# Kernel tuning notes

Measured on AMD Instinct MI355X. Metric: run time of the kernel, lower is better.

Reference implementation:

```python
import jax, jax.numpy as jnp
import numpy as np

V, BLOCK, L, H, E = 1000, 1024, 8, 16, 1024
D = E // H
HID = 4 * E
B, S = 4, 1024
NEG = -1e9


def setup_inputs() -> dict:
    key = jax.random.key(0)
    ks = jax.random.split(key, 10)
    s = 0.02
    rn = lambda k, shp: jax.random.normal(k, shp, jnp.float32) * s
    return dict(
        idx=jax.random.randint(ks[0], (B, S), 0, V),
        wte=rn(ks[1], (V, E)),
        wpe=rn(ks[2], (BLOCK, E)),
        ln1_w=jnp.ones((L, E), jnp.float32), ln1_b=jnp.zeros((L, E), jnp.float32),
        qkv_w=rn(ks[3], (L, E, 3 * E)), qkv_b=jnp.zeros((L, 3 * E), jnp.float32),
        out_w=rn(ks[4], (L, E, E)), out_b=jnp.zeros((L, E), jnp.float32),
        ln2_w=jnp.ones((L, E), jnp.float32), ln2_b=jnp.zeros((L, E), jnp.float32),
        fc1_w=rn(ks[5], (L, E, HID)), fc1_b=jnp.zeros((L, HID), jnp.float32),
        fc2_w=rn(ks[6], (L, HID, E)), fc2_b=jnp.zeros((L, E), jnp.float32),
        lnf_w=jnp.ones((E,), jnp.float32), lnf_b=jnp.zeros((E,), jnp.float32),
        head_w=rn(ks[7], (E, V)), head_b=jnp.zeros((V,), jnp.float32),
    )


def _ln(x, w, b):
    m = x.mean(-1, keepdims=True)
    v = x.var(-1, keepdims=True)
    return (x - m) / jnp.sqrt(v + 1e-5) * w + b


def _block(x, p):
    (ln1_w, ln1_b, qkv_w, qkv_b, out_w, out_b,
     ln2_w, ln2_b, fc1_w, fc1_b, fc2_w, fc2_b) = p
    b, s, _ = x.shape
    # --- causal self-attention ---
    h = _ln(x, ln1_w, ln1_b)
    qkv = h @ qkv_w + qkv_b                           # [b, s, 3E]
    q, k, v = jnp.split(qkv, 3, axis=-1)
    q = q.reshape(b, s, H, D)
    k = k.reshape(b, s, H, D)
    v = v.reshape(b, s, H, D)
    att = jnp.einsum('bqhd,bkhd->bhqk', q, k) / np.sqrt(D).astype(np.float32)
    mask = jnp.tril(jnp.ones((s, s), bool))
    att = jnp.where(mask, att, NEG)
    att = jax.nn.softmax(att, axis=-1)
    y = jnp.einsum('bhqk,bkhd->bqhd', att, v).reshape(b, s, E)
    x = x + (y @ out_w + out_b)
    # --- MLP ---
    h = _ln(x, ln2_w, ln2_b)
    h = jax.nn.gelu(h @ fc1_w + fc1_b, approximate=False)
    x = x + (h @ fc2_w + fc2_b)
    return x


def reference(idx, wte, wpe, ln1_w, ln1_b, qkv_w, qkv_b, out_w, out_b,
              ln2_w, ln2_b, fc1_w, fc1_b, fc2_w, fc2_b, lnf_w, lnf_b,
              head_w, head_b):
    s = idx.shape[1]
    x = wte[idx] + wpe[:s]                            # [B, S, E]
    layer_params = (ln1_w, ln1_b, qkv_w, qkv_b, out_w, out_b,
                    ln2_w, ln2_b, fc1_w, fc1_b, fc2_w, fc2_b)
    def step(x, p):
        return _block(x, p), None
    x, _ = jax.lax.scan(step, x, layer_params)
    x = _ln(x, lnf_w, lnf_b)
    logits = x @ head_w + head_b                      # [B, S, V]
    return logits
```

## Files before the change

### kernel.cpp

```cpp
#include <hip/hip_runtime.h>
#include <math.h>


typedef unsigned short u16;
typedef unsigned int u32;
typedef __attribute__((ext_vector_type(4))) float f32x4;
typedef __attribute__((ext_vector_type(8))) __bf16 bf16x8;
typedef __attribute__((ext_vector_type(8))) u16 u16x8;
typedef __attribute__((ext_vector_type(4))) u16 u16x4;

#define E 1024
#define HID 4096
#define NH 16
#define HD 64
#define SEQ 1024
#define NB 4
#define NL 8
#define MTOK 4096
#define VOC 1000

#define VMCNT(n) asm volatile("s_waitcnt vmcnt(" #n ")" ::: "memory")

__device__ __forceinline__ u16 f2bf(float f){
  u32 u = __float_as_uint(f);
  u32 r = (u + 0x7fffu + ((u >> 16) & 1u)) >> 16;
  return (u16)r;
}
__device__ __forceinline__ float bf2f(u16 b){
  return __uint_as_float((u32)b << 16);
}
__device__ __forceinline__ bf16x8 ld_bf8(const u16* p){
  return *reinterpret_cast<const bf16x8*>(p);
}
__device__ __forceinline__ bf16x8 as_bf(u16x8 v){
  return __builtin_bit_cast(bf16x8, v);
}

__device__ __forceinline__ void gload16(const void* g, void* l){
  __builtin_amdgcn_global_load_lds(
      (const __attribute__((address_space(1))) void*)g,
      (__attribute__((address_space(3))) void*)l, 16, 0, 0);
}

__global__ __launch_bounds__(256) void embed_kernel(
    const int* __restrict__ idx, const float* __restrict__ wte,
    const float* __restrict__ wpe, u16* __restrict__ x)
{
  int tok = blockIdx.x, tid = threadIdx.x;
  int id = idx[tok];
  int s = tok & (SEQ - 1);
  f32x4 a = *reinterpret_cast<const f32x4*>(&wte[(size_t)id * E + tid * 4]);
  f32x4 p = *reinterpret_cast<const f32x4*>(&wpe[(size_t)s * E + tid * 4]);
  u16x4 r;
  #pragma unroll
  for (int j = 0; j < 4; j++) r[j] = f2bf(a[j] + p[j]);
  *reinterpret_cast<u16x4*>(&x[(size_t)tok * E + tid * 4]) = r;
}

__global__ __launch_bounds__(256) void ln_kernel(
    const u16* __restrict__ x, const float* __restrict__ w,
    const float* __restrict__ b, u16* __restrict__ h)
{
  int row = blockIdx.x, tid = threadIdx.x;
  u16x4 xv = *reinterpret_cast<const u16x4*>(&x[(size_t)row * E + tid * 4]);
  f32x4 v;
  #pragma unroll
  for (int j = 0; j < 4; j++) v[j] = bf2f(xv[j]);
  float s = v[0] + v[1] + v[2] + v[3];
  float q = v[0]*v[0] + v[1]*v[1] + v[2]*v[2] + v[3]*v[3];
  #pragma unroll
  for (int mm = 1; mm < 64; mm <<= 1){
    s += __shfl_xor(s, mm);
    q += __shfl_xor(q, mm);
  }
  __shared__ float red[8];
  int wv = tid >> 6;
  if ((tid & 63) == 0){ red[wv] = s; red[4 + wv] = q; }
  __syncthreads();
  s = red[0] + red[1] + red[2] + red[3];
  q = red[4] + red[5] + red[6] + red[7];
  float mean = s * (1.0f / E);
  float var = q * (1.0f / E) - mean * mean;
  float rstd = rsqrtf(var + 1e-5f);
  f32x4 wv4 = *reinterpret_cast<const f32x4*>(w + tid * 4);
  f32x4 bv4 = *reinterpret_cast<const f32x4*>(b + tid * 4);
  u16x4 o;
  #pragma unroll
  for (int j = 0; j < 4; j++)
    o[j] = f2bf((v[j] - mean) * rstd * wv4[j] + bv4[j]);
  *reinterpret_cast<u16x4*>(&h[(size_t)row * E + tid * 4]) = o;
}

__global__ __launch_bounds__(256) void lnadd_kernel(
    u16* __restrict__ x, const u16* __restrict__ p,
    const float* __restrict__ w, const float* __restrict__ b,
    u16* __restrict__ h)
{
  int row = blockIdx.x, tid = threadIdx.x;
  u16* xr = x + (size_t)row * E + tid * 4;
  u16x4 xv = *reinterpret_cast<const u16x4*>(xr);
  u16x4 pv = *reinterpret_cast<const u16x4*>(&p[(size_t)row * E + tid * 4]);
  f32x4 v;
  u16x4 nx;
  #pragma unroll
  for (int j = 0; j < 4; j++){
    v[j] = bf2f(xv[j]) + bf2f(pv[j]);
    nx[j] = f2bf(v[j]);
  }
  *reinterpret_cast<u16x4*>(xr) = nx;
  float s = v[0] + v[1] + v[2] + v[3];
  float q = v[0]*v[0] + v[1]*v[1] + v[2]*v[2] + v[3]*v[3];
  #pragma unroll
  for (int mm = 1; mm < 64; mm <<= 1){
    s += __shfl_xor(s, mm);
    q += __shfl_xor(q, mm);
  }
  __shared__ float red[8];
  int wv = tid >> 6;
  if ((tid & 63) == 0){ red[wv] = s; red[4 + wv] = q; }
  __syncthreads();
  s = red[0] + red[1] + red[2] + red[3];
  q = red[4] + red[5] + red[6] + red[7];
  float mean = s * (1.0f / E);
  float var = q * (1.0f / E) - mean * mean;
  float rstd = rsqrtf(var + 1e-5f);
  f32x4 wv4 = *reinterpret_cast<const f32x4*>(w + tid * 4);
  f32x4 bv4 = *reinterpret_cast<const f32x4*>(b + tid * 4);
  u16x4 o;
  #pragma unroll
  for (int j = 0; j < 4; j++)
    o[j] = f2bf((v[j] - mean) * rstd * wv4[j] + bv4[j]);
  *reinterpret_cast<u16x4*>(&h[(size_t)row * E + tid * 4]) = o;
}

__global__ __launch_bounds__(256) void wconv4_kernel(
    const float* __restrict__ qw, const float* __restrict__ ow,
    const float* __restrict__ f1, const float* __restrict__ f2,
    u16* __restrict__ dq, u16* __restrict__ d_unused, u16* __restrict__ d1,
    u16* __restrict__ d2, u16* __restrict__ dw_out)
{
  const int bid = blockIdx.x, tid = threadIdx.x;
  const float* W; u16* Wt; int K, Nsrc, nx, base;
  if (bid < 768)      { W = qw; Wt = dq;     K = 1024; Nsrc = 3072; nx = 48; base = 0; }
  else if (bid < 1024){ W = ow; Wt = dw_out; K = 1024; Nsrc = 1024; nx = 16; base = 768; }
  else if (bid < 2048){ W = f1; Wt = d1;     K = 1024; Nsrc = 4096; nx = 64; base = 1024; }
  else                { W = f2; Wt = d2;     K = 4096; Nsrc = 1024; nx = 16; base = 2048; }
  const int t = bid - base;
  const int n0 = (t % nx) * 64, k0 = (t / nx) * 64;

  __shared__ float T[64][65];
  const int c = (tid & 15) * 4, rbase = tid >> 4;
  #pragma unroll
  for (int p = 0; p < 4; p++){
    int r = rbase + p * 16;
    f32x4 v = *reinterpret_cast<const f32x4*>(&W[(size_t)(k0 + r) * Nsrc + n0 + c]);
    T[r][c] = v[0]; T[r][c+1] = v[1]; T[r][c+2] = v[2]; T[r][c+3] = v[3];
  }
  __syncthreads();
  const int nr = tid >> 2, ks = (tid & 3) * 16;
  u16x8 o0, o1;
  #pragma unroll
  for (int i = 0; i < 8; i++){
    o0[i] = f2bf(T[ks + i][nr]);
    o1[i] = f2bf(T[ks + 8 + i][nr]);
  }
  u16* dst = &Wt[(size_t)(n0 + nr) * K + k0 + ks];
  *reinterpret_cast<u16x8*>(dst) = o0;
  *reinterpret_cast<u16x8*>(dst + 8) = o1;
}

__global__ __launch_bounds__(256) void wconv_kernel(
    const float* __restrict__ W, u16* __restrict__ Wt,
    int K, int Nsrc, int N)
{
  __shared__ float T[64][65];
  const int tid = threadIdx.x;
  const int n0 = blockIdx.x * 64, k0 = blockIdx.y * 64;
  const int c = (tid & 15) * 4, rbase = tid >> 4;
  #pragma unroll
  for (int p = 0; p < 4; p++){
    int r = rbase + p * 16;
    #pragma unroll
    for (int j = 0; j < 4; j++){
      int n = n0 + c + j;
      T[r][c + j] = (n < Nsrc) ? W[(size_t)(k0 + r) * Nsrc + n] : 0.0f;
    }
  }
  __syncthreads();
  const int nr = tid >> 2, ks = (tid & 3) * 16;
  u16x8 o0, o1;
  #pragma unroll
  for (int i = 0; i < 8; i++){
    o0[i] = f2bf(T[ks + i][nr]);
    o1[i] = f2bf(T[ks + 8 + i][nr]);
  }
  u16* dst = &Wt[(size_t)(n0 + nr) * K + k0 + ks];
  *reinterpret_cast<u16x8*>(dst) = o0;
  *reinterpret_cast<u16x8*>(dst + 8) = o1;
}

enum { EPI_BF16 = 0, EPI_GELU = 1, EPI_OUT = 3 };

template<int EPI, int NW, int NWX, int FM, int FN, int MINW>
__global__ __launch_bounds__(NW * 64, MINW) void gemm2_kernel(
    const u16* __restrict__ A, const u16* __restrict__ Wt,
    const float* __restrict__ bias, void* __restrict__ outp,
    int M, int N, int K)
{
  constexpr int BM = FM * 16 * (NW / NWX);
  constexpr int BN = FN * 16 * NWX;
  constexpr int SLOT = (BM + BN) * 32;
  constexpr int GROUPS = (BM + BN) / 16;
  constexpr bool UNI = (GROUPS % NW) == 0;
  constexpr int RPW = UNI ? GROUPS / NW : 0;
  constexpr int NS = 4;
  extern __shared__ u16 lds[];

  const int tid = threadIdx.x;
  const int lane = tid & 63, w = tid >> 6;
  const int l15 = lane & 15, g = lane >> 4;
  const int wr = w / NWX, wc = w % NWX;
  const int wrbase = wr * FM * 16, wcbase = wc * FN * 16;

  const int nwgx = gridDim.x;
  const int bid = blockIdx.y * nwgx + blockIdx.x;
  const int cpx = (nwgx * gridDim.y) >> 3;
  const int swz = (bid & 7) * cpx + (bid >> 3);
  const int bm = (swz / nwgx) * BM, bn = (swz % nwgx) * BN;

  const u16* Abase = A + (size_t)bm * K;
  const u16* Bbase = Wt + (size_t)bn * K;

  f32x4 acc[FM][FN];
  #pragma unroll
  for (int i = 0; i < FM; i++)
    #pragma unroll
    for (int j = 0; j < FN; j++)
      acc[i][j] = f32x4{0.f, 0.f, 0.f, 0.f};

  const int lr = lane >> 2, ps = lane & 3;
  const int ss = ps ^ ((lane >> 4) & 3);
  auto STAGE = [&](int s, int cc){
    const int k0 = cc * 32;
    u16* As = lds + s * SLOT;
    u16* Bs = As + BM * 32;
    if constexpr (UNI){
      #pragma unroll
      for (int j = 0; j < RPW; j++){
        int base = (w * RPW + j) * 16;
        if (base < BM){
          gload16(&Abase[(size_t)(base + lr) * K + k0 + ss * 8], As + base * 32);
        } else {
          int rb = base - BM;
          gload16(&Bbase[(size_t)(rb + lr) * K + k0 + ss * 8], Bs + rb * 32);
        }
      }
    } else {
      static_assert(BM == 256 && BN == 192, "non-uniform path is specialized");
      if (w < 4){
        #pragma unroll
        for (int j = 0; j < 4; j++){
          int base = (w * 4 + j) * 16;
          gload16(&Abase[(size_t)(base + lr) * K + k0 + ss * 8], As + base * 32);
        }
      } else {
        #pragma unroll
        for (int j = 0; j < 3; j++){
          int rb = ((w - 4) * 3 + j) * 16;
          gload16(&Bbase[(size_t)(rb + lr) * K + k0 + ss * 8], Bs + rb * 32);
        }
      }
    }
  };
  auto WAIT1 = [&](){
    if constexpr (UNI){
      static_assert(!UNI || RPW == 4 || RPW == 3, "vmcnt literal covers RPW 3/4");
      if constexpr (RPW == 4) { VMCNT(4); } else { VMCNT(3); }
    } else {
      if (w < 4) { VMCNT(4); } else { VMCNT(3); }
    }
  };

  const int nt = K >> 5;
  STAGE(0, 0); STAGE(1, 1); STAGE(2, 2);
  WAIT1();
  __builtin_amdgcn_sched_barrier(0);
  __builtin_amdgcn_s_barrier();
  __builtin_amdgcn_sched_barrier(0);

  int sl = 0;
  for (int c = 0; c < nt; c++){
    const u16* As = lds + sl * SLOT;
    const u16* Bs = As + BM * 32;
    bf16x8 af[FM], bf[FN];
    const int rsw = (g ^ (l15 >> 2)) * 8;
    #pragma unroll
    for (int mf = 0; mf < FM; mf++)
      af[mf] = ld_bf8(&As[(wrbase + mf * 16 + l15) * 32 + rsw]);
    #pragma unroll
    for (int nf = 0; nf < FN; nf++)
      bf[nf] = ld_bf8(&Bs[(wcbase + nf * 16 + l15) * 32 + rsw]);
    __builtin_amdgcn_sched_barrier(0);
    if (c + 2 <= nt - 1) { WAIT1(); } else { VMCNT(0); }
    __builtin_amdgcn_sched_barrier(0);
    __builtin_amdgcn_s_barrier();
    __builtin_amdgcn_sched_barrier(0);
    __builtin_amdgcn_s_setprio(1);
    #pragma unroll
    for (int mf = 0; mf < FM; mf++)
      #pragma unroll
      for (int nf = 0; nf < FN; nf++)
        acc[mf][nf] = __builtin_amdgcn_mfma_f32_16x16x32_bf16(
            af[mf], bf[nf], acc[mf][nf], 0, 0, 0);
    __builtin_amdgcn_s_setprio(0);
    if (c + 3 < nt){
      int s2 = sl + 3; if (s2 >= NS) s2 -= NS;
      STAGE(s2, c + 3);
    }
    sl++; if (sl >= NS) sl -= NS;
  }

  #pragma unroll
  for (int mf = 0; mf < FM; mf++){
    #pragma unroll
    for (int nf = 0; nf < FN; nf++){
      int col = bn + wcbase + nf * 16 + l15;
      float bv = bias[col];
      #pragma unroll
      for (int r = 0; r < 4; r++){
        int row = bm + wrbase + mf * 16 + g * 4 + r;
        float v = acc[mf][nf][r] + bv;
        if constexpr (EPI == EPI_BF16){
          ((u16*)outp)[(size_t)row * N + col] = f2bf(v);
        } else if constexpr (EPI == EPI_GELU){
          ((u16*)outp)[(size_t)row * N + col] =
              f2bf(0.5f * v * (1.0f + erff(v * 0.70710678118654752f)));
        } else {
          if (col < VOC)
            ((float*)outp)[(size_t)row * VOC + col] = v;
        }
      }
    }
  }
}

__global__ __launch_bounds__(512) void attn_kernel(
    const u16* __restrict__ qkv, u16* __restrict__ y)
{
  __shared__ u16 Kl[64 * 64];
  __shared__ u16 Vt[64 * 72];
  __shared__ u16 Pl[8 * 16 * 72];
  const int pr = blockIdx.x, hh = blockIdx.y, b = blockIdx.z;
  const int tid = threadIdx.x;
  const int lane = tid & 63, w = tid >> 6;
  const int w4 = w & 3, wg = w >> 2;
  const int l15 = lane & 15, g = lane >> 4;
  const size_t tokbase = (size_t)b * SEQ;
  const int qs0 = (wg == 0 ? pr : 7 - pr) * 64;
  const int qs1 = (wg == 0 ? 15 - pr : 8 + pr) * 64;
  const int qstart[2] = { qs0, qs1 };

  int qbase[2], dt[2];
  u16x8 q0[2], q1[2];
  f32x4 o[2][4];
  float m[2][4], llp[2][4];
  #pragma unroll
  for (int st = 0; st < 2; st++){
    qbase[st] = qstart[st] + w4 * 16;
    dt[st] = qbase[st] >> 6;
    const u16* qp = &qkv[(tokbase + qbase[st] + l15) * (3 * E) + hh * HD];
    u16x8 ra = *reinterpret_cast<const u16x8*>(&qp[g * 8]);
    u16x8 rb = *reinterpret_cast<const u16x8*>(&qp[32 + g * 8]);
    #pragma unroll
    for (int j = 0; j < 8; j++){
      q0[st][j] = f2bf(bf2f(ra[j]) * 0.125f);
      q1[st][j] = f2bf(bf2f(rb[j]) * 0.125f);
    }
    #pragma unroll
    for (int dc = 0; dc < 4; dc++) o[st][dc] = f32x4{0.f, 0.f, 0.f, 0.f};
    #pragma unroll
    for (int r = 0; r < 4; r++){ m[st][r] = -1e30f; llp[st][r] = 0.f; }
  }

  u16* Pw = &Pl[w * 16 * 72];
  const int T = 16 - pr;

  for (int t = 0; t < T; t++){
    const int k0 = t * 64;
    __syncthreads();
    {
      int row = w * 8 + (lane >> 3);
      int sl = lane & 7;
      const u16* src = &qkv[(tokbase + k0 + row) * (3 * E) + E + hh * HD
                            + ((sl ^ (row & 7)) * 8)];
      gload16(src, &Kl[w * 512]);
    }
    {
      int d0 = (tid & 15) * 4;
      int s  = (tid >> 4) & 15;
      int mh = tid >> 8;
      int kA = s + 32 * mh;
      const u16* vpA = &qkv[(tokbase + k0 + kA) * (3 * E) + 2 * E + hh * HD + d0];
      const u16* vpB = vpA + 16 * (3 * E);
      u16x4 va = *reinterpret_cast<const u16x4*>(vpA);
      u16x4 vb = *reinterpret_cast<const u16x4*>(vpB);
      #pragma unroll
      for (int i = 0; i < 4; i++)
        *reinterpret_cast<u32*>(&Vt[(d0 + i) * 72 + 4 * s + 2 * mh]) =
            (u32)va[i] | ((u32)vb[i] << 16);
    }
    __syncthreads();

    #pragma unroll
    for (int st = 0; st < 2; st++){
      if (t > dt[st]) continue;
      const bool diag = (t == dt[st]);
      f32x4 s[4];
      #pragma unroll
      for (int kg = 0; kg < 4; kg++){
        int key = kg * 16 + l15;
        const u16* kb = &Kl[key * 64];
        bf16x8 k0f = ld_bf8(&kb[(g ^ (key & 7)) * 8]);
        bf16x8 k1f = ld_bf8(&kb[((4 + g) ^ (key & 7)) * 8]);
        f32x4 z = f32x4{0.f, 0.f, 0.f, 0.f};
        z = __builtin_amdgcn_mfma_f32_16x16x32_bf16(as_bf(q0[st]), k0f, z, 0, 0, 0);
        z = __builtin_amdgcn_mfma_f32_16x16x32_bf16(as_bf(q1[st]), k1f, z, 0, 0, 0);
        s[kg] = z;
      }
      if (diag){
        #pragma unroll
        for (int kg = 0; kg < 4; kg++){
          int key = k0 + kg * 16 + l15;
          #pragma unroll
          for (int r = 0; r < 4; r++){
            int q = qbase[st] + g * 4 + r;
            s[kg][r] = (key <= q) ? s[kg][r] : -1e9f;
          }
        }
      }
      float lmax[4];
      bool need = false;
      #pragma unroll
      for (int r = 0; r < 4; r++){
        lmax[r] = fmaxf(fmaxf(s[0][r], s[1][r]), fmaxf(s[2][r], s[3][r]));
        need = need || (lmax[r] > m[st][r] + 8.0f);
      }
      if (__any(need)){
        #pragma unroll
        for (int r = 0; r < 4; r++){
          float x = lmax[r];
          x = fmaxf(x, __shfl_xor(x, 1));
          x = fmaxf(x, __shfl_xor(x, 2));
          x = fmaxf(x, __shfl_xor(x, 4));
          x = fmaxf(x, __shfl_xor(x, 8));
          float mn = fmaxf(m[st][r], x);
          float al = __expf(m[st][r] - mn);
          m[st][r] = mn;
          llp[st][r] *= al;
          #pragma unroll
          for (int dc = 0; dc < 4; dc++) o[st][dc][r] *= al;
        }
      }
      #pragma unroll
      for (int r = 0; r < 4; r++){
        float p0 = __expf(s[0][r] - m[st][r]);
        float p1 = __expf(s[1][r] - m[st][r]);
        float p2 = __expf(s[2][r] - m[st][r]);
        float p3 = __expf(s[3][r] - m[st][r]);
        llp[st][r] += (p0 + p1) + (p2 + p3);
        u16x4 pp = { f2bf(p0), f2bf(p1), f2bf(p2), f2bf(p3) };
        *reinterpret_cast<u16x4*>(&Pw[(g * 4 + r) * 72 + 4 * l15]) = pp;
      }
      bf16x8 pa0 = ld_bf8(&Pw[l15 * 72 + g * 8]);
      bf16x8 pa1 = ld_bf8(&Pw[l15 * 72 + 32 + g * 8]);
      #pragma unroll
      for (int dc = 0; dc < 4; dc++){
        bf16x8 v0 = ld_bf8(&Vt[(dc * 16 + l15) * 72 + g * 8]);
        bf16x8 v1 = ld_bf8(&Vt[(dc * 16 + l15) * 72 + 32 + g * 8]);
        o[st][dc] = __builtin_amdgcn_mfma_f32_16x16x32_bf16(pa0, v0, o[st][dc], 0, 0, 0);
        o[st][dc] = __builtin_amdgcn_mfma_f32_16x16x32_bf16(pa1, v1, o[st][dc], 0, 0, 0);
      }
    }
  }

  #pragma unroll
  for (int st = 0; st < 2; st++){
    #pragma unroll
    for (int r = 0; r < 4; r++){
      float rs = llp[st][r];
      rs += __shfl_xor(rs, 1);
      rs += __shfl_xor(rs, 2);
      rs += __shfl_xor(rs, 4);
      rs += __shfl_xor(rs, 8);
      float inv = 1.0f / rs;
      int row = qbase[st] + g * 4 + r;
      #pragma unroll
      for (int dc = 0; dc < 4; dc++){
        int col = hh * HD + dc * 16 + l15;
        y[(tokbase + row) * E + col] = f2bf(o[st][dc][r] * inv);
      }
    }
  }
}

__global__ __launch_bounds__(256) void biaspad_kernel(
    const float* __restrict__ hb, float* __restrict__ bpad)
{
  int i = blockIdx.x * 256 + threadIdx.x;
  if (i < 1024) bpad[i] = (i < VOC) ? hb[i] : 0.0f;
}

extern "C" void kernel_launch(void* const* d_in, const int* in_sizes, int n_in,
                              void* d_out, int out_size, void* d_ws, size_t ws_size,
                              hipStream_t stream)
{
  const int*   idx    = (const int*)  d_in[0];
  const float* wte    = (const float*)d_in[1];
  const float* wpe    = (const float*)d_in[2];
  const float* ln1_w  = (const float*)d_in[3];
  const float* ln1_b  = (const float*)d_in[4];
  const float* qkv_w  = (const float*)d_in[5];
  const float* qkv_b  = (const float*)d_in[6];
  const float* out_w  = (const float*)d_in[7];
  const float* out_b  = (const float*)d_in[8];
  const float* ln2_w  = (const float*)d_in[9];
  const float* ln2_b  = (const float*)d_in[10];
  const float* fc1_w  = (const float*)d_in[11];
  const float* fc1_b  = (const float*)d_in[12];
  const float* fc2_w  = (const float*)d_in[13];
  const float* fc2_b  = (const float*)d_in[14];
  const float* lnf_w  = (const float*)d_in[15];
  const float* lnf_b  = (const float*)d_in[16];
  const float* head_w = (const float*)d_in[17];
  const float* head_b = (const float*)d_in[18];

  char* ws = (char*)d_ws;
  u16*   x    = (u16*)  (ws + 0);
  u16*   h    = (u16*)  (ws + 8388608);
  u16*   qkvb = (u16*)  (ws + 16777216);
  u16*   y    = (u16*)  (ws + 41943040);
  u16*   g    = (u16*)  (ws + 50331648);
  u16*   wq   = (u16*)  (ws + 83886080);
  u16*   wo   = (u16*)  (ws + 90177536);
  u16*   w1   = (u16*)  (ws + 92274688);
  u16*   w2   = (u16*)  (ws + 100663296);
  u16*   wh   = (u16*)  (ws + 109051904);
  float* hbp  = (float*)(ws + 111149056);
  u16*   p    = (u16*)  (ws + 111153152);

  constexpr int LDS_QKV = 4 * (448 * 32) * 2;
  constexpr int LDS_BIG = 4 * (512 * 32) * 2;
  constexpr int LDS_SML = 4 * (192 * 32) * 2;
  hipFuncSetAttribute((const void*)gemm2_kernel<EPI_BF16, 8, 4, 8, 3, 2>,
                      hipFuncAttributeMaxDynamicSharedMemorySize, LDS_QKV);
  hipFuncSetAttribute((const void*)gemm2_kernel<EPI_GELU, 8, 4, 8, 4, 2>,
                      hipFuncAttributeMaxDynamicSharedMemorySize, LDS_BIG);
  hipFuncSetAttribute((const void*)gemm2_kernel<EPI_BF16, 4, 2, 4, 2, 2>,
                      hipFuncAttributeMaxDynamicSharedMemorySize, LDS_SML);
  hipFuncSetAttribute((const void*)gemm2_kernel<EPI_OUT, 4, 2, 4, 2, 2>,
                      hipFuncAttributeMaxDynamicSharedMemorySize, LDS_SML);

  embed_kernel<<<MTOK, 256, 0, stream>>>(idx, wte, wpe, x);
  biaspad_kernel<<<4, 256, 0, stream>>>(head_b, hbp);

  for (int l = 0; l < NL; l++){
    if (l == 0){
      ln_kernel<<<MTOK, 256, 0, stream>>>(x, ln1_w, ln1_b, h);
    } else {
      lnadd_kernel<<<MTOK, 256, 0, stream>>>(x, p, ln1_w + l * E, ln1_b + l * E, h);
    }
    wconv4_kernel<<<3072, 256, 0, stream>>>(
        qkv_w + (size_t)l * E * 3 * E, out_w + (size_t)l * E * E,
        fc1_w + (size_t)l * E * HID, fc2_w + (size_t)l * HID * E,
        wq, nullptr, w1, w2, wo);
    gemm2_kernel<EPI_BF16, 8, 4, 8, 3, 2><<<dim3(16, 16), 512, LDS_QKV, stream>>>(
        h, wq, qkv_b + (size_t)l * 3 * E, qkvb, MTOK, 3 * E, E);
    attn_kernel<<<dim3(4, NH, NB), 512, 0, stream>>>(qkvb, y);
    gemm2_kernel<EPI_BF16, 4, 2, 4, 2, 2><<<dim3(16, 32), 256, LDS_SML, stream>>>(
        y, wo, out_b + (size_t)l * E, p, MTOK, E, E);
    lnadd_kernel<<<MTOK, 256, 0, stream>>>(x, p, ln2_w + l * E, ln2_b + l * E, h);
    gemm2_kernel<EPI_GELU, 8, 4, 8, 4, 2><<<dim3(16, 16), 512, LDS_BIG, stream>>>(
        h, w1, fc1_b + (size_t)l * HID, g, MTOK, HID, E);
    gemm2_kernel<EPI_BF16, 4, 2, 4, 2, 2><<<dim3(16, 32), 256, LDS_SML, stream>>>(
        g, w2, fc2_b + (size_t)l * E, p, MTOK, E, HID);
  }
  lnadd_kernel<<<MTOK, 256, 0, stream>>>(x, p, lnf_w, lnf_b, h);
  wconv_kernel<<<dim3(16, 16), 256, 0, stream>>>(head_w, wh, E, VOC, E);
  gemm2_kernel<EPI_OUT, 4, 2, 4, 2, 2><<<dim3(16, 32), 256, LDS_SML, stream>>>(
      h, wh, hbp, (float*)d_out, MTOK, E, E);
}
```

Baseline: 1.771 ms.

## Double-buffer K/V tiles in attention kernel to overlap loads with compute

Adds a second LDS buffer for K and transposed V so the next key tile's global loads are issued before computing on the current tile. The V transpose store to LDS happens after the MFMA work, followed by a single barrier per iteration instead of two. This is meant to hide global memory latency behind the QK/PV compute. The cost is doubled LDS for K/V, which may lower occupancy, and extra registers held across the compute for the prefetched V values.

```diff
diff --git a/kernel.cpp b/kernel.cpp
--- a/kernel.cpp
+++ b/kernel.cpp
@@ -20,6 +20,7 @@
 #define VOC 1000
 
 #define VMCNT(n) asm volatile("s_waitcnt vmcnt(" #n ")" ::: "memory")
+#define LGKMCNT0() asm volatile("s_waitcnt lgkmcnt(0)" ::: "memory")
 
 __device__ __forceinline__ u16 f2bf(float f){
   u32 u = __float_as_uint(f);
@@ -347,8 +348,8 @@
 __global__ __launch_bounds__(512) void attn_kernel(
     const u16* __restrict__ qkv, u16* __restrict__ y)
 {
-  __shared__ u16 Kl[64 * 64];
-  __shared__ u16 Vt[64 * 72];
+  __shared__ u16 Kl[2][64 * 64];
+  __shared__ u16 Vt[2][64 * 72];
   __shared__ u16 Pl[8 * 16 * 72];
   const int pr = blockIdx.x, hh = blockIdx.y, b = blockIdx.z;
   const int tid = threadIdx.x;
@@ -360,6 +361,14 @@
   const int qs1 = (wg == 0 ? 15 - pr : 8 + pr) * 64;
   const int qstart[2] = { qs0, qs1 };
 
+  const int krow = w * 8 + (lane >> 3);
+  const int kslot = ((lane & 7) ^ (krow & 7)) * 8;
+  const int vd0 = (tid & 15) * 4;
+  const int vs  = (tid >> 4) & 15;
+  const int vmh = tid >> 8;
+  const int vcpos = 4 * vs + 2 * vmh;
+  const int vkA = vs + 32 * vmh;
+
   int qbase[2], dt[2];
   u16x8 q0[2], q1[2];
   f32x4 o[2][4];
@@ -385,31 +394,32 @@
   u16* Pw = &Pl[w * 16 * 72];
   const int T = 16 - pr;
 
+  {
+    gload16(&qkv[(tokbase + krow) * (3 * E) + E + hh * HD + kslot], &Kl[0][w * 512]);
+    const u16* vpA = &qkv[(tokbase + vkA) * (3 * E) + 2 * E + hh * HD + vd0];
+    u16x4 va = *reinterpret_cast<const u16x4*>(vpA);
+    u16x4 vb = *reinterpret_cast<const u16x4*>(vpA + 16 * (3 * E));
+    VMCNT(0);
+    #pragma unroll
+    for (int i = 0; i < 4; i++)
+      *reinterpret_cast<u32*>(&Vt[0][(vd0 + i) * 72 + vcpos]) =
+          (u32)va[i] | ((u32)vb[i] << 16);
+  }
+  __syncthreads();
+
+  int buf = 0;
   for (int t = 0; t < T; t++){
     const int k0 = t * 64;
-    __syncthreads();
-    {
-      int row = w * 8 + (lane >> 3);
-      int sl = lane & 7;
-      const u16* src = &qkv[(tokbase + k0 + row) * (3 * E) + E + hh * HD
-                            + ((sl ^ (row & 7)) * 8)];
-      gload16(src, &Kl[w * 512]);
-    }
-    {
-      int d0 = (tid & 15) * 4;
-      int s  = (tid >> 4) & 15;
-      int mh = tid >> 8;
-      int kA = s + 32 * mh;
-      const u16* vpA = &qkv[(tokbase + k0 + kA) * (3 * E) + 2 * E + hh * HD + d0];
-      const u16* vpB = vpA + 16 * (3 * E);
-      u16x4 va = *reinterpret_cast<const u16x4*>(vpA);
-      u16x4 vb = *reinterpret_cast<const u16x4*>(vpB);
-      #pragma unroll
-      for (int i = 0; i < 4; i++)
-        *reinterpret_cast<u32*>(&Vt[(d0 + i) * 72 + 4 * s + 2 * mh]) =
-            (u32)va[i] | ((u32)vb[i] << 16);
-    }
-    __syncthreads();
+    const bool more = (t + 1 < T);
+    u16x4 va, vb;
+    if (more){
+      const int k0n = k0 + 64;
+      gload16(&qkv[(tokbase + k0n + krow) * (3 * E) + E + hh * HD + kslot],
+              &Kl[buf ^ 1][w * 512]);
+      const u16* vpA = &qkv[(tokbase + k0n + vkA) * (3 * E) + 2 * E + hh * HD + vd0];
+      va = *reinterpret_cast<const u16x4*>(vpA);
+      vb = *reinterpret_cast<const u16x4*>(vpA + 16 * (3 * E));
+    }
 
     #pragma unroll
     for (int st = 0; st < 2; st++){
@@ -419,7 +429,7 @@
       #pragma unroll
       for (int kg = 0; kg < 4; kg++){
         int key = kg * 16 + l15;
-        const u16* kb = &Kl[key * 64];
+        const u16* kb = &Kl[buf][key * 64];
         bf16x8 k0f = ld_bf8(&kb[(g ^ (key & 7)) * 8]);
         bf16x8 k1f = ld_bf8(&kb[((4 + g) ^ (key & 7)) * 8]);
         f32x4 z = f32x4{0.f, 0.f, 0.f, 0.f};
@@ -448,12 +458,12 @@
       if (__any(need)){
         #pragma unroll
         for (int r = 0; r < 4; r++){
-          float x = lmax[r];
-          x = fmaxf(x, __shfl_xor(x, 1));
-          x = fmaxf(x, __shfl_xor(x, 2));
-          x = fmaxf(x, __shfl_xor(x, 4));
-          x = fmaxf(x, __shfl_xor(x, 8));
-          float mn = fmaxf(m[st][r], x);
+          float xx = lmax[r];
+          xx = fmaxf(xx, __shfl_xor(xx, 1));
+          xx = fmaxf(xx, __shfl_xor(xx, 2));
+          xx = fmaxf(xx, __shfl_xor(xx, 4));
+          xx = fmaxf(xx, __shfl_xor(xx, 8));
+          float mn = fmaxf(m[st][r], xx);
           float al = __expf(m[st][r] - mn);
           m[st][r] = mn;
           llp[st][r] *= al;
@@ -475,12 +485,25 @@
       bf16x8 pa1 = ld_bf8(&Pw[l15 * 72 + 32 + g * 8]);
       #pragma unroll
       for (int dc = 0; dc < 4; dc++){
-        bf16x8 v0 = ld_bf8(&Vt[(dc * 16 + l15) * 72 + g * 8]);
-        bf16x8 v1 = ld_bf8(&Vt[(dc * 16 + l15) * 72 + 32 + g * 8]);
+        bf16x8 v0 = ld_bf8(&Vt[buf][(dc * 16 + l15) * 72 + g * 8]);
+        bf16x8 v1 = ld_bf8(&Vt[buf][(dc * 16 + l15) * 72 + 32 + g * 8]);
         o[st][dc] = __builtin_amdgcn_mfma_f32_16x16x32_bf16(pa0, v0, o[st][dc], 0, 0, 0);
         o[st][dc] = __builtin_amdgcn_mfma_f32_16x16x32_bf16(pa1, v1, o[st][dc], 0, 0, 0);
       }
     }
+
+    if (more){
+      VMCNT(0);
+      #pragma unroll
+      for (int i = 0; i < 4; i++)
+        *reinterpret_cast<u32*>(&Vt[buf ^ 1][(vd0 + i) * 72 + vcpos]) =
+            (u32)va[i] | ((u32)vb[i] << 16);
+    }
+    LGKMCNT0();
+    __builtin_amdgcn_sched_barrier(0);
+    __builtin_amdgcn_s_barrier();
+    __builtin_amdgcn_sched_barrier(0);
+    buf ^= 1;
   }
 
   #pragma unroll
```

Result: no change. 1.762 ms, median of 2 (-0.5%).
